# Kernel tuning notes

Hardware: AMD Instinct MI355X
Metric: run time of the kernel (lower is better)

The kernel has to match this reference:

```python
import jax, jax.numpy as jnp
import numpy as np

B, P, C, H, W = 32, 6, 2048, 16, 8   # batch, parts-per-image, feat_dim, feature map
HEADS, DHEAD, LAYERS = 4, 512, 2      # GATv2: hidden = feat_dim // heads
N = B * P                             # graph nodes


def setup_inputs() -> dict:
    key = jax.random.key(0)
    ks = jax.random.split(key, 6)
    return {
        "features": jax.random.normal(ks[0], (B, P * C, H, W), jnp.float32),
        "img_num_ps": jax.random.randint(ks[1], (B,), 1, P + 1, jnp.int32),
        "Wl": jax.random.normal(ks[2], (LAYERS, HEADS, C, DHEAD), jnp.float32) * 0.02,
        "bl": jnp.zeros((LAYERS, HEADS, DHEAD), jnp.float32),
        "Wr": jax.random.normal(ks[3], (LAYERS, HEADS, C, DHEAD), jnp.float32) * 0.02,
        "br": jnp.zeros((LAYERS, HEADS, DHEAD), jnp.float32),
        "att": jax.random.normal(ks[4], (LAYERS, HEADS, DHEAD), jnp.float32) * 0.05,
        "gat_bias": jnp.zeros((LAYERS, HEADS * DHEAD), jnp.float32),
        "bn_gamma": jnp.ones((C,), jnp.float32),
        "bn_mean": jnp.zeros((C,), jnp.float32),
        "bn_var": jnp.ones((C,), jnp.float32),
    }


def _intra_mask(img_num_ps):
    # instance one-hot (blocks of 6) + one_hot_refine zeroing, then adj = oh @ oh.T == 1
    node = jnp.arange(N)
    valid = (node % P) < img_num_ps[node // P]
    inst = node // P
    adj = (inst[:, None] == inst[None, :]) & valid[:, None] & valid[None, :]
    # PyG GATv2Conv: remove existing self loops then add self loops for all nodes
    return adj | jnp.eye(N, dtype=bool)


def _gatv2(x, mask, Wl, bl, Wr, br, att, gat_bias):
    NEG = jnp.float32(-1e30)
    for l in range(LAYERS):
        xl = jnp.einsum('nc,hcd->nhd', x, Wl[l]) + bl[l]  # source (lin_l)
        xr = jnp.einsum('nc,hcd->nhd', x, Wr[l]) + br[l]  # target (lin_r)
        z = jax.nn.leaky_relu(xr[:, None] + xl[None, :], 0.2)   # [i,j,h,d]
        s = jnp.einsum('ijhd,hd->hij', z, att[l])               # [h,i,j]
        s = jnp.where(mask[None], s, NEG)
        alpha = jax.nn.softmax(s, axis=-1)                      # softmax over sources j
        out = jnp.einsum('hij,jhd->ihd', alpha, xl)
        x = out.reshape(N, HEADS * DHEAD) + gat_bias[l]
        if l < LAYERS - 1:
            x = jax.nn.elu(x)
    return x


def reference(features, img_num_ps, Wl, bl, Wr, br, att, gat_bias, bn_gamma, bn_mean, bn_var):
    # torch.chunk(features, 6, dim=1) -> cat(dim=0): chunk-major node ordering
    parts = features.reshape(B, P, C, H, W).transpose(1, 0, 2, 3, 4).reshape(N, C, H, W)
    pool_feat = parts.mean(axis=(2, 3))                     # GlobalAvgPool -> [N, C]
    mask = _intra_mask(img_num_ps)
    graph_feat = _gatv2(pool_feat, mask, Wl, bl, Wr, br, att, gat_bias) + pool_feat
    # chunk(graph_feat, 6, dim=0) stacked on dim=1, mean over parts -> [B, C]
    gfa = graph_feat.reshape(P, B, C).transpose(1, 0, 2).mean(axis=1)
    # BN neck, eval mode, frozen bias = 0
    return bn_gamma * (gfa - bn_mean) / jnp.sqrt(bn_var + 1e-5)
```

## Files before the change

kernel.cpp:

```cpp
#include <hip/hip_runtime.h>
#include <hip/hip_bf16.h>


#define NNODES 192
#define CFEAT  2048

typedef __attribute__((ext_vector_type(8))) short bf16x8;
typedef __attribute__((ext_vector_type(4))) float f32x4;

__device__ inline unsigned f2bf(float f) {
    union { float f; unsigned u; } v; v.f = f;
    unsigned u = v.u;
    u += 0x7FFFu + ((u >> 16) & 1u);
    return u >> 16;
}
__device__ inline float bf2f(unsigned short u) {
    union { unsigned u; float f; } v; v.u = (unsigned)u << 16;
    return v.f;
}

__global__ __launch_bounds__(256) void pool_kernel(const float* __restrict__ F,
                                                   float* __restrict__ POOL,
                                                   unsigned short* __restrict__ POOLB) {
    int wave = threadIdx.x >> 6, lane = threadIdx.x & 63;
    #pragma unroll
    for (int it = 0; it < 12; ++it) {
        int dr = blockIdx.x * 4 + wave + it * 16384;
        int r0 = dr * 2;
        int n = r0 >> 11, c0 = r0 & 2047;
        int p = n >> 5, b = n & 31;
        const float* src = F + (((size_t)b * 12288 + (size_t)p * 2048 + c0) << 7);
        float4 v = *(const float4*)(src + (lane << 2));
        float acc = (v.x + v.y) + (v.z + v.w);
        acc += __shfl_down(acc, 16);
        acc += __shfl_down(acc, 8);
        acc += __shfl_down(acc, 4);
        acc += __shfl_down(acc, 2);
        acc += __shfl_down(acc, 1);
        if ((lane & 31) == 0) {
            int r = r0 + (lane >> 5);
            float m = acc * (1.0f / 128.0f);
            POOL[r] = m;
            POOLB[r] = (unsigned short)f2bf(m);
        }
    }
}

__global__ __launch_bounds__(256) void gemm_kernel(
    const unsigned short* __restrict__ X,
    const float* __restrict__ WL,
    const float* __restrict__ WR,
    unsigned short* __restrict__ P) {
    int bx = blockIdx.x, sk = blockIdx.y;
    int t = threadIdx.x, w = t >> 6, l = t & 63;
    int lr = l & 15, lg = l >> 4;
    int kbeg = sk << 8;

    const float* Wb = (bx >= 32 ? WR : WL)
                    + (size_t)((bx & 31) >> 3) * (2048 * 512)
                    + ((bx & 7) << 6) + (w << 4) + lr;
    const unsigned short* Xp = X + (size_t)lr * 2048 + kbeg + lg * 8;

    f32x4 acc[12];
    #pragma unroll
    for (int i = 0; i < 12; ++i) acc[i] = {0.f, 0.f, 0.f, 0.f};

    for (int step = 0; step < 8; ++step) {
        int k0 = step << 5;
        const float* wp = Wb + (size_t)(kbeg + k0 + lg * 8) * 512;
        float b0 = wp[0],        b1 = wp[512],      b2 = wp[2 * 512], b3 = wp[3 * 512];
        float b4 = wp[4 * 512],  b5 = wp[5 * 512],  b6 = wp[6 * 512], b7 = wp[7 * 512];
        uint4 bb;
        bb.x = f2bf(b0) | (f2bf(b1) << 16);
        bb.y = f2bf(b2) | (f2bf(b3) << 16);
        bb.z = f2bf(b4) | (f2bf(b5) << 16);
        bb.w = f2bf(b6) | (f2bf(b7) << 16);
        bf16x8 bfr = __builtin_bit_cast(bf16x8, bb);
        #pragma unroll
        for (int fi = 0; fi < 12; ++fi) {
            bf16x8 af = *(const bf16x8*)(Xp + (size_t)fi * 16 * 2048 + k0);
            acc[fi] = __builtin_amdgcn_mfma_f32_16x16x32_bf16(af, bfr, acc[fi], 0, 0, 0);
        }
    }

    unsigned short* Pp = P + (size_t)sk * (192 * 4096)
                       + (size_t)(lg * 4) * 4096 + (bx << 6) + (w << 4) + lr;
    #pragma unroll
    for (int fi = 0; fi < 12; ++fi)
        #pragma unroll
        for (int j = 0; j < 4; ++j)
            Pp[(size_t)(fi * 16 + j) * 4096] = (unsigned short)f2bf(acc[fi][j]);
}

template <int LAYER>
__global__ __launch_bounds__(256) void attn_kernel(
    const unsigned short* __restrict__ P,
    const float* __restrict__ BL,
    const float* __restrict__ BR,
    const float* __restrict__ ATT,
    const float* __restrict__ GBIAS,
    const int* __restrict__ NPS,
    const float* __restrict__ POOL,
    float* __restrict__ OUTF,
    unsigned short* __restrict__ OUTB) {
    __shared__ float xls[6][512];
    __shared__ float xrs[6][512];
    __shared__ float atts[512];
    __shared__ float s_sm[6][6];
    __shared__ float alpha[6][6];

    int g = blockIdx.x, h = blockIdx.y;
    int tid = threadIdx.x;
    int cnt = NPS[g];

    for (int idx = tid; idx < 6 * 512; idx += 256) {
        int q = idx >> 9, d = idx & 511;
        int col = h * 512 + d;
        size_t base = (size_t)(g * 6 + q) * 4096 + col;
        float sl = BL[col], sr = BR[col];
        #pragma unroll
        for (int sk = 0; sk < 8; ++sk) {
            const unsigned short* Ps = P + (size_t)sk * (192 * 4096) + base;
            sl += bf2f(Ps[0]);
            sr += bf2f(Ps[2048]);
        }
        xls[q][d] = sl;
        xrs[q][d] = sr;
    }
    for (int d = tid; d < 512; d += 256) atts[d] = ATT[h * 512 + d];
    __syncthreads();

    int wv = tid >> 6, lane = tid & 63;
    for (int p = wv; p < 36; p += 4) {
        int i = p / 6, j = p % 6;
        float acc = 0.f;
        #pragma unroll
        for (int u = 0; u < 8; ++u) {
            int d = lane + u * 64;
            float v = xrs[i][d] + xls[j][d];
            v = (v >= 0.f) ? v : 0.2f * v;
            acc = fmaf(atts[d], v, acc);
        }
        #pragma unroll
        for (int off = 32; off; off >>= 1) acc += __shfl_down(acc, off);
        if (lane == 0) s_sm[i][j] = acc;
    }
    __syncthreads();

    if (tid < 6) {
        int i = tid;
        bool iv = i < cnt;
        float mx;
        if (iv) {
            mx = -1e30f;
            for (int j = 0; j < cnt; ++j) mx = fmaxf(mx, s_sm[i][j]);
        } else {
            mx = s_sm[i][i];
        }
        float e[6], sum = 0.f;
        for (int j = 0; j < 6; ++j) {
            bool nb = iv ? (j < cnt) : (j == i);
            e[j] = nb ? expf(s_sm[i][j] - mx) : 0.f;
            sum += e[j];
        }
        float inv = 1.f / sum;
        for (int j = 0; j < 6; ++j) alpha[i][j] = e[j] * inv;
    }
    __syncthreads();

    for (int idx = tid; idx < 6 * 512; idx += 256) {
        int q = idx >> 9, d = idx & 511;
        float acc = 0.f;
        #pragma unroll
        for (int j = 0; j < 6; ++j) acc = fmaf(alpha[q][j], xls[j][d], acc);
        int col = h * 512 + d;
        size_t off = (size_t)(g * 6 + q) * 2048 + col;
        float v = acc + GBIAS[col];
        if (LAYER == 0) {
            v = (v > 0.f) ? v : expm1f(v);
            OUTB[off] = (unsigned short)f2bf(v);
        } else {
            OUTF[off] = v + POOL[off];
        }
    }
}

__global__ __launch_bounds__(256) void final_kernel(
    const float* __restrict__ GF, const float* __restrict__ GAMMA,
    const float* __restrict__ MEAN, const float* __restrict__ VAR,
    float* __restrict__ OUTP) {
    int idx = blockIdx.x * 256 + threadIdx.x;
    int c = idx & 2047, b = idx >> 11;
    float acc = 0.f;
    #pragma unroll
    for (int p = 0; p < 6; ++p) acc += GF[(size_t)(p * 32 + b) * 2048 + c];
    acc *= (1.f / 6.f);
    OUTP[idx] = GAMMA[c] * (acc - MEAN[c]) * rsqrtf(VAR[c] + 1e-5f);
}

extern "C" void kernel_launch(void* const* d_in, const int* in_sizes, int n_in,
                              void* d_out, int out_size, void* d_ws, size_t ws_size,
                              hipStream_t stream) {
    const float* F     = (const float*)d_in[0];
    const int*   nps   = (const int*)d_in[1];
    const float* Wl    = (const float*)d_in[2];
    const float* bl    = (const float*)d_in[3];
    const float* Wr    = (const float*)d_in[4];
    const float* br    = (const float*)d_in[5];
    const float* att   = (const float*)d_in[6];
    const float* gb    = (const float*)d_in[7];
    const float* gamma = (const float*)d_in[8];
    const float* mean  = (const float*)d_in[9];
    const float* var   = (const float*)d_in[10];
    float* out = (float*)d_out;
    float* wsf = (float*)d_ws;

    const size_t SZ = (size_t)NNODES * CFEAT;
    float* pool = wsf;
    float* gf   = wsf + SZ;
    unsigned short* P     = (unsigned short*)(wsf + 2 * SZ);
    unsigned short* poolb = (unsigned short*)(wsf + 10 * SZ);
    unsigned short* x1b   = (unsigned short*)(wsf + 11 * SZ);

    const size_t WOFF = 4ull * 2048 * 512;

    pool_kernel<<<dim3(4096), dim3(256), 0, stream>>>(F, pool, poolb);

    gemm_kernel<<<dim3(64, 8), dim3(256), 0, stream>>>(poolb, Wl, Wr, P);
    attn_kernel<0><<<dim3(32, 4), dim3(256), 0, stream>>>(P, bl, br, att, gb, nps,
                                                          nullptr, nullptr, x1b);

    gemm_kernel<<<dim3(64, 8), dim3(256), 0, stream>>>(x1b, Wl + WOFF, Wr + WOFF, P);
    attn_kernel<1><<<dim3(32, 4), dim3(256), 0, stream>>>(P, bl + 2048, br + 2048,
                                                          att + 2048, gb + 2048,
                                                          nps, pool, gf, nullptr);

    final_kernel<<<dim3(256), dim3(256), 0, stream>>>(gf, gamma, mean, var, out);
}
```

Measured before the change: 148.3 us.

## Drop split-K in projection GEMM, prefetch weights, write fp32 with bias

The projection GEMM no longer uses an 8-way split-K with bf16 partial sums. It now runs 128 blocks, each covering the full K=2048 for 32 output columns and all 192 rows, with a 4-deep software register prefetch of weight and activation fragments. Bias is added in the GEMM epilogue and fp32 results go straight to Y, so the attention kernel reads one value instead of summing eight partials. This removes the partial-sum traffic and the reduction, but cuts the grid from 512 to 128 blocks and lengthens each block's serial K loop, which lowers parallelism on a large GPU.

```diff
diff --git a/kernel.cpp b/kernel.cpp
--- a/kernel.cpp
+++ b/kernel.cpp
@@ -13,10 +13,6 @@
     unsigned u = v.u;
     u += 0x7FFFu + ((u >> 16) & 1u);
     return u >> 16;
-}
-__device__ inline float bf2f(unsigned short u) {
-    union { unsigned u; float f; } v; v.u = (unsigned)u << 16;
-    return v.f;
 }
 
 __global__ __launch_bounds__(256) void pool_kernel(const float* __restrict__ F,
@@ -50,53 +46,86 @@
     const unsigned short* __restrict__ X,
     const float* __restrict__ WL,
     const float* __restrict__ WR,
-    unsigned short* __restrict__ P) {
-    int bx = blockIdx.x, sk = blockIdx.y;
+    const float* __restrict__ BL,
+    const float* __restrict__ BR,
+    float* __restrict__ Y) {
+    int ct = blockIdx.x;
     int t = threadIdx.x, w = t >> 6, l = t & 63;
     int lr = l & 15, lg = l >> 4;
-    int kbeg = sk << 8;
-
-    const float* Wb = (bx >= 32 ? WR : WL)
-                    + (size_t)((bx & 31) >> 3) * (2048 * 512)
-                    + ((bx & 7) << 6) + (w << 4) + lr;
-    const unsigned short* Xp = X + (size_t)lr * 2048 + kbeg + lg * 8;
-
-    f32x4 acc[12];
-    #pragma unroll
-    for (int i = 0; i < 12; ++i) acc[i] = {0.f, 0.f, 0.f, 0.f};
-
-    for (int step = 0; step < 8; ++step) {
-        int k0 = step << 5;
-        const float* wp = Wb + (size_t)(kbeg + k0 + lg * 8) * 512;
-        float b0 = wp[0],        b1 = wp[512],      b2 = wp[2 * 512], b3 = wp[3 * 512];
-        float b4 = wp[4 * 512],  b5 = wp[5 * 512],  b6 = wp[6 * 512], b7 = wp[7 * 512];
-        uint4 bb;
-        bb.x = f2bf(b0) | (f2bf(b1) << 16);
-        bb.y = f2bf(b2) | (f2bf(b3) << 16);
-        bb.z = f2bf(b4) | (f2bf(b5) << 16);
-        bb.w = f2bf(b6) | (f2bf(b7) << 16);
-        bf16x8 bfr = __builtin_bit_cast(bf16x8, bb);
-        #pragma unroll
-        for (int fi = 0; fi < 12; ++fi) {
-            bf16x8 af = *(const bf16x8*)(Xp + (size_t)fi * 16 * 2048 + k0);
-            acc[fi] = __builtin_amdgcn_mfma_f32_16x16x32_bf16(af, bfr, acc[fi], 0, 0, 0);
-        }
-    }
-
-    unsigned short* Pp = P + (size_t)sk * (192 * 4096)
-                       + (size_t)(lg * 4) * 4096 + (bx << 6) + (w << 4) + lr;
-    #pragma unroll
-    for (int fi = 0; fi < 12; ++fi)
-        #pragma unroll
-        for (int j = 0; j < 4; ++j)
-            Pp[(size_t)(fi * 16 + j) * 4096] = (unsigned short)f2bf(acc[fi][j]);
+
+    int bcol = ((ct & 63) << 5) + lr;
+    int head = bcol >> 9, dcol = bcol & 511;
+    const float* Wb = ((ct >= 64) ? WR : WL)
+                    + (size_t)head * (2048 * 512) + dcol;
+    const unsigned short* Xp = X + (size_t)(48 * w + lr) * 2048 + lg * 8;
+
+    f32x4 acc[3][2];
+    #pragma unroll
+    for (int i = 0; i < 3; ++i)
+        #pragma unroll
+        for (int j = 0; j < 2; ++j) acc[i][j] = {0.f, 0.f, 0.f, 0.f};
+
+    float  fb[4][16];
+    bf16x8 fa[4][3];
+
+#define LOAD_SLOT(slot, step)                                                 \
+    {                                                                         \
+        const float* wp = Wb + (size_t)(((step) << 5) + lg * 8) * 512;        \
+        _Pragma("unroll")                                                     \
+        for (int j = 0; j < 8; ++j) {                                         \
+            fb[slot][j]     = wp[(size_t)j * 512];                            \
+            fb[slot][8 + j] = wp[(size_t)j * 512 + 16];                       \
+        }                                                                     \
+        const unsigned short* xp = Xp + ((step) << 5);                        \
+        fa[slot][0] = *(const bf16x8*)(xp);                                   \
+        fa[slot][1] = *(const bf16x8*)(xp + 16 * 2048);                       \
+        fa[slot][2] = *(const bf16x8*)(xp + 32 * 2048);                       \
+    }
+
+    #pragma unroll
+    for (int s = 0; s < 4; ++s) LOAD_SLOT(s, s)
+
+    for (int it = 0; it < 64; it += 4) {
+        #pragma unroll
+        for (int u = 0; u < 4; ++u) {
+            int s = it + u;
+            bf16x8 bf0, bf1;
+            #pragma unroll
+            for (int j = 0; j < 8; ++j) {
+                bf0[j] = (short)__builtin_bit_cast(unsigned short,
+                              __float2bfloat16(fb[u][j]));
+                bf1[j] = (short)__builtin_bit_cast(unsigned short,
+                              __float2bfloat16(fb[u][8 + j]));
+            }
+            acc[0][0] = __builtin_amdgcn_mfma_f32_16x16x32_bf16(fa[u][0], bf0, acc[0][0], 0, 0, 0);
+            acc[0][1] = __builtin_amdgcn_mfma_f32_16x16x32_bf16(fa[u][0], bf1, acc[0][1], 0, 0, 0);
+            acc[1][0] = __builtin_amdgcn_mfma_f32_16x16x32_bf16(fa[u][1], bf0, acc[1][0], 0, 0, 0);
+            acc[1][1] = __builtin_amdgcn_mfma_f32_16x16x32_bf16(fa[u][1], bf1, acc[1][1], 0, 0, 0);
+            acc[2][0] = __builtin_amdgcn_mfma_f32_16x16x32_bf16(fa[u][2], bf0, acc[2][0], 0, 0, 0);
+            acc[2][1] = __builtin_amdgcn_mfma_f32_16x16x32_bf16(fa[u][2], bf1, acc[2][1], 0, 0, 0);
+            if (s + 4 < 64) LOAD_SLOT(u, s + 4)
+        }
+    }
+#undef LOAD_SLOT
+
+    float b0 = ((ct >= 64) ? BR : BL)[bcol];
+    float b1 = ((ct >= 64) ? BR : BL)[bcol + 16];
+    int ycol = ((ct >= 64) ? 2048 : 0) + bcol;
+    #pragma unroll
+    for (int fi = 0; fi < 3; ++fi) {
+        int rbase = 48 * w + 16 * fi + lg * 4;
+        #pragma unroll
+        for (int j = 0; j < 4; ++j) {
+            float* dst = Y + (size_t)(rbase + j) * 4096 + ycol;
+            dst[0]  = acc[fi][0][j] + b0;
+            dst[16] = acc[fi][1][j] + b1;
+        }
+    }
 }
 
 template <int LAYER>
 __global__ __launch_bounds__(256) void attn_kernel(
-    const unsigned short* __restrict__ P,
-    const float* __restrict__ BL,
-    const float* __restrict__ BR,
+    const float* __restrict__ Y,
     const float* __restrict__ ATT,
     const float* __restrict__ GBIAS,
     const int* __restrict__ NPS,
@@ -115,17 +144,9 @@
 
     for (int idx = tid; idx < 6 * 512; idx += 256) {
         int q = idx >> 9, d = idx & 511;
-        int col = h * 512 + d;
-        size_t base = (size_t)(g * 6 + q) * 4096 + col;
-        float sl = BL[col], sr = BR[col];
-        #pragma unroll
-        for (int sk = 0; sk < 8; ++sk) {
-            const unsigned short* Ps = P + (size_t)sk * (192 * 4096) + base;
-            sl += bf2f(Ps[0]);
-            sr += bf2f(Ps[2048]);
-        }
-        xls[q][d] = sl;
-        xrs[q][d] = sr;
+        size_t off = (size_t)(g * 6 + q) * 4096 + h * 512 + d;
+        xls[q][d] = Y[off];
+        xrs[q][d] = Y[off + 2048];
     }
     for (int d = tid; d < 512; d += 256) atts[d] = ATT[h * 512 + d];
     __syncthreads();
@@ -218,21 +239,21 @@
     const size_t SZ = (size_t)NNODES * CFEAT;
     float* pool = wsf;
     float* gf   = wsf + SZ;
-    unsigned short* P     = (unsigned short*)(wsf + 2 * SZ);
-    unsigned short* poolb = (unsigned short*)(wsf + 10 * SZ);
-    unsigned short* x1b   = (unsigned short*)(wsf + 11 * SZ);
+    float* Y    = wsf + 2 * SZ;
+    unsigned short* poolb = (unsigned short*)(wsf + 4 * SZ);
+    unsigned short* x1b   = (unsigned short*)(wsf + 5 * SZ);
 
     const size_t WOFF = 4ull * 2048 * 512;
 
     pool_kernel<<<dim3(4096), dim3(256), 0, stream>>>(F, pool, poolb);
 
-    gemm_kernel<<<dim3(64, 8), dim3(256), 0, stream>>>(poolb, Wl, Wr, P);
-    attn_kernel<0><<<dim3(32, 4), dim3(256), 0, stream>>>(P, bl, br, att, gb, nps,
+    gemm_kernel<<<dim3(128), dim3(256), 0, stream>>>(poolb, Wl, Wr, bl, br, Y);
+    attn_kernel<0><<<dim3(32, 4), dim3(256), 0, stream>>>(Y, att, gb, nps,
                                                           nullptr, nullptr, x1b);
 
-    gemm_kernel<<<dim3(64, 8), dim3(256), 0, stream>>>(x1b, Wl + WOFF, Wr + WOFF, P);
-    attn_kernel<1><<<dim3(32, 4), dim3(256), 0, stream>>>(P, bl + 2048, br + 2048,
-                                                          att + 2048, gb + 2048,
+    gemm_kernel<<<dim3(128), dim3(256), 0, stream>>>(x1b, Wl + WOFF, Wr + WOFF,
+                                                     bl + 2048, br + 2048, Y);
+    attn_kernel<1><<<dim3(32, 4), dim3(256), 0, stream>>>(Y, att + 2048, gb + 2048,
                                                           nps, pool, gf, nullptr);
 
     final_kernel<<<dim3(256), dim3(256), 0, stream>>>(gf, gamma, mean, var, out);
```

Result: no change. 150.4 us (+1.4%).
